# Performance work log

Hardware: AMD Instinct MI355X
Metric: run time of the kernel (lower is better)

## Reference

```python
import jax, jax.numpy as jnp
import numpy as np

N = 8192
F_IN = 256
F_OUT = 128
ALPHA = 0.2  # leaky relu negative slope


def _leaky(x):
    return jnp.where(x >= 0, x, ALPHA * x)


def setup_inputs() -> dict:
    key = jax.random.key(0)
    ks = jax.random.split(key, 12)
    nodes = jax.random.normal(ks[0], (N, F_IN), dtype=jnp.float32)
    adj = (jax.random.uniform(ks[1], (N, N)) < 0.05).astype(jnp.float32)
    adj = jnp.maximum(adj, jnp.eye(N, dtype=jnp.float32))
    s = 0.02
    W1 = jax.random.normal(ks[2], (F_IN, F_OUT), dtype=jnp.float32) * s
    b1 = jnp.zeros((F_OUT,), jnp.float32)
    W2 = jax.random.normal(ks[3], (F_OUT, F_OUT), dtype=jnp.float32) * s
    b2 = jnp.zeros((F_OUT,), jnp.float32)
    W3 = jax.random.normal(ks[4], (F_OUT, F_OUT), dtype=jnp.float32) * s
    b3 = jnp.zeros((F_OUT,), jnp.float32)
    W4 = jax.random.normal(ks[5], (F_OUT, F_OUT), dtype=jnp.float32) * s
    b4 = jnp.zeros((F_OUT,), jnp.float32)
    a_w = jax.random.normal(ks[6], (2 * F_OUT,), dtype=jnp.float32) * s
    a_b = jnp.zeros((), jnp.float32)
    return {"nodes": nodes, "adj": adj, "W1": W1, "b1": b1, "W2": W2, "b2": b2,
            "W3": W3, "b3": b3, "W4": W4, "b4": b4, "a_w": a_w, "a_b": a_b}


def reference(nodes, adj, W1, b1, W2, b2, W3, b3, W4, b4, a_w, a_b):
    # 4-layer linear stack
    h = jax.nn.relu(nodes @ W1 + b1)
    h = jax.nn.relu(h @ W2 + b2)
    h = jax.nn.relu(h @ W3 + b3)
    h = h @ W4 + b4  # (N, F_OUT)
    # a([h_i, h_j]) is linear -> split into src/dst components instead of
    # materializing the (N, N, 2F) repeat+cat tensor; identical math.
    a1, a2 = a_w[:F_OUT], a_w[F_OUT:]
    s_src = h @ a1  # (N,)
    s_dst = h @ a2  # (N,)
    e = _leaky(s_src[:, None] + s_dst[None, :] + a_b)  # (N, N)
    e = jnp.where(adj >= 0.5, e, -jnp.inf)
    attention = jax.nn.softmax(e, axis=1)
    # dropout is identity in eval mode
    return _leaky(attention @ h)  # (N, F_OUT)
```

## Files before the change

### kernel.cpp

```cpp
#include <hip/hip_runtime.h>
#include <hip/hip_bf16.h>

#define N_NODES 8192
#define F_IN    256
#define F_OUT   128
#define CHUNK   512
#define NCH     4
#define CCAP    768

typedef float f4v __attribute__((ext_vector_type(4)));

__device__ __forceinline__ float leaky(float x) { return x >= 0.f ? x : 0.2f * x; }

__global__ __launch_bounds__(256) void mlp_fused(
    const float* __restrict__ nodes,
    const float* __restrict__ W1, const float* __restrict__ b1,
    const float* __restrict__ W2, const float* __restrict__ b2,
    const float* __restrict__ W3, const float* __restrict__ b3,
    const float* __restrict__ W4, const float* __restrict__ b4,
    const float* __restrict__ aw,
    float* __restrict__ h_out, float* __restrict__ ss, float* __restrict__ sd) {
  __shared__ float As[32][36];
  __shared__ float Ws[32][128];
  __shared__ float hTa[128][36];
  __shared__ float hTb[128][36];
  __shared__ float awS[2 * F_OUT];
  __shared__ float sred[2][8][32];

  const int tid = threadIdx.x;
  const int bm0 = blockIdx.x * 32;
  const int mt = tid >> 5;
  const int nt = tid & 31;
  const int ar = tid >> 3;
  const int ac = tid & 7;

  awS[tid] = aw[tid];

  float acc[4][4] = {};

  for (int k0 = 0; k0 < F_IN; k0 += 32) {
    const float4 av = *(const float4*)(nodes + (size_t)(bm0 + ar) * F_IN + k0 + ac * 4);
    float4 wv[4];
#pragma unroll
    for (int i = 0; i < 4; ++i) {
      const int kk = i * 8 + (tid >> 5);
      wv[i] = *(const float4*)(W1 + (size_t)(k0 + kk) * F_OUT + nt * 4);
    }
    __syncthreads();
    As[ac * 4 + 0][ar] = av.x;
    As[ac * 4 + 1][ar] = av.y;
    As[ac * 4 + 2][ar] = av.z;
    As[ac * 4 + 3][ar] = av.w;
#pragma unroll
    for (int i = 0; i < 4; ++i) {
      const int kk = i * 8 + (tid >> 5);
      *(float4*)&Ws[kk][nt * 4] = wv[i];
    }
    __syncthreads();
#pragma unroll
    for (int k = 0; k < 32; ++k) {
      const float4 a = *(const float4*)&As[k][mt * 4];
      const float4 w = *(const float4*)&Ws[k][nt * 4];
      acc[0][0] += a.x * w.x; acc[0][1] += a.x * w.y; acc[0][2] += a.x * w.z; acc[0][3] += a.x * w.w;
      acc[1][0] += a.y * w.x; acc[1][1] += a.y * w.y; acc[1][2] += a.y * w.z; acc[1][3] += a.y * w.w;
      acc[2][0] += a.z * w.x; acc[2][1] += a.z * w.y; acc[2][2] += a.z * w.z; acc[2][3] += a.z * w.w;
      acc[3][0] += a.w * w.x; acc[3][1] += a.w * w.y; acc[3][2] += a.w * w.z; acc[3][3] += a.w * w.w;
    }
  }
  {
    const float4 bv = *(const float4*)(b1 + nt * 4);
#pragma unroll
    for (int i = 0; i < 4; ++i) {
      hTa[nt * 4 + 0][mt * 4 + i] = fmaxf(acc[i][0] + bv.x, 0.f);
      hTa[nt * 4 + 1][mt * 4 + i] = fmaxf(acc[i][1] + bv.y, 0.f);
      hTa[nt * 4 + 2][mt * 4 + i] = fmaxf(acc[i][2] + bv.z, 0.f);
      hTa[nt * 4 + 3][mt * 4 + i] = fmaxf(acc[i][3] + bv.w, 0.f);
    }
  }

  const float* Wl[3] = {W2, W3, W4};
  const float* bl[3] = {b2, b3, b4};
  float* hin = &hTa[0][0];
  float* hout = &hTb[0][0];
  for (int l = 0; l < 3; ++l) {
#pragma unroll
    for (int i = 0; i < 4; ++i)
#pragma unroll
      for (int j = 0; j < 4; ++j) acc[i][j] = 0.f;
    for (int k0 = 0; k0 < F_OUT; k0 += 32) {
      float4 wv[4];
#pragma unroll
      for (int i = 0; i < 4; ++i) {
        const int kk = i * 8 + (tid >> 5);
        wv[i] = *(const float4*)(Wl[l] + (size_t)(k0 + kk) * F_OUT + nt * 4);
      }
      __syncthreads();
#pragma unroll
      for (int i = 0; i < 4; ++i) {
        const int kk = i * 8 + (tid >> 5);
        *(float4*)&Ws[kk][nt * 4] = wv[i];
      }
      __syncthreads();
#pragma unroll
      for (int k = 0; k < 32; ++k) {
        const float4 a = *(const float4*)(hin + (size_t)(k0 + k) * 36 + mt * 4);
        const float4 w = *(const float4*)&Ws[k][nt * 4];
        acc[0][0] += a.x * w.x; acc[0][1] += a.x * w.y; acc[0][2] += a.x * w.z; acc[0][3] += a.x * w.w;
        acc[1][0] += a.y * w.x; acc[1][1] += a.y * w.y; acc[1][2] += a.y * w.z; acc[1][3] += a.y * w.w;
        acc[2][0] += a.z * w.x; acc[2][1] += a.z * w.y; acc[2][2] += a.z * w.z; acc[2][3] += a.z * w.w;
        acc[3][0] += a.w * w.x; acc[3][1] += a.w * w.y; acc[3][2] += a.w * w.z; acc[3][3] += a.w * w.w;
      }
    }
    const float4 bv = *(const float4*)(bl[l] + nt * 4);
    const bool relu = (l < 2);
#pragma unroll
    for (int i = 0; i < 4; ++i) {
      float o0 = acc[i][0] + bv.x, o1 = acc[i][1] + bv.y;
      float o2 = acc[i][2] + bv.z, o3 = acc[i][3] + bv.w;
      if (relu) {
        o0 = fmaxf(o0, 0.f); o1 = fmaxf(o1, 0.f);
        o2 = fmaxf(o2, 0.f); o3 = fmaxf(o3, 0.f);
      }
      hout[(size_t)(nt * 4 + 0) * 36 + mt * 4 + i] = o0;
      hout[(size_t)(nt * 4 + 1) * 36 + mt * 4 + i] = o1;
      hout[(size_t)(nt * 4 + 2) * 36 + mt * 4 + i] = o2;
      hout[(size_t)(nt * 4 + 3) * 36 + mt * 4 + i] = o3;
    }
    float* t = hin; hin = hout; hout = t;
  }
  __syncthreads();

  {
    const int r = tid & 31;
    const int fg = tid >> 5;
    float s1 = 0.f, s2 = 0.f;
#pragma unroll
    for (int i = 0; i < 16; ++i) {
      const int f = fg * 16 + i;
      const float hv = hin[(size_t)f * 36 + r];
      s1 += hv * awS[f];
      s2 += hv * awS[F_OUT + f];
    }
    sred[0][fg][r] = s1;
    sred[1][fg][r] = s2;
  }
  {
    const int r = tid >> 3;
    const int c = tid & 7;
    float4 o[4];
#pragma unroll
    for (int u = 0; u < 4; ++u) {
      o[u].x = hin[(size_t)(c * 16 + u * 4 + 0) * 36 + r];
      o[u].y = hin[(size_t)(c * 16 + u * 4 + 1) * 36 + r];
      o[u].z = hin[(size_t)(c * 16 + u * 4 + 2) * 36 + r];
      o[u].w = hin[(size_t)(c * 16 + u * 4 + 3) * 36 + r];
    }
    float4* dst = (float4*)(h_out + (size_t)(bm0 + r) * F_OUT + c * 16);
#pragma unroll
    for (int u = 0; u < 4; ++u) dst[u] = o[u];
  }
  __syncthreads();
  if (tid < 32) {
    float s1 = 0.f, s2 = 0.f;
#pragma unroll
    for (int g = 0; g < 8; ++g) { s1 += sred[0][g][tid]; s2 += sred[1][g][tid]; }
    ss[bm0 + tid] = s1;
    sd[bm0 + tid] = s2;
  }
}

__global__ __launch_bounds__(512) void attn_kernel(const float* __restrict__ adj,
                                                   const float* __restrict__ h,
                                                   const float* __restrict__ s_src,
                                                   const float* __restrict__ s_dst,
                                                   const float* __restrict__ ab_ptr,
                                                   float* __restrict__ out) {
  __shared__ float2 lst[2][CCAP];
  __shared__ int   cnt[NCH];
  __shared__ float accs[16][32][4];
  __shared__ float red_sum[8];

  const int tid = threadIdx.x;
  const int lane = tid & 63;
  const int wid = tid >> 6;
  const int row = blockIdx.x;
  if (tid < NCH) cnt[tid] = 0;

  const float sbase = s_src[row] + ab_ptr[0];
  const f4v* arow = (const f4v*)(adj + (size_t)row * N_NODES);
  const float4* sd4 = (const float4*)s_dst;
  const float4* h4 = (const float4*)h;
  const unsigned long long lt = (1ull << lane) - 1ull;
  const int g = tid >> 5;
  const int q = tid & 31;

  f4v av = __builtin_nontemporal_load(arow + tid);
  float4 sv = sd4[tid];

  float lsum = 0.f;
  float4 acc = {0.f, 0.f, 0.f, 0.f};
  __syncthreads();

#pragma unroll
  for (int c = 0; c < NCH; ++c) {
    const f4v av_c = av;
    const float4 sv_c = sv;
    if (c + 1 < NCH) {
      av = __builtin_nontemporal_load(arow + (c + 1) * CHUNK + tid);
      sv = sd4[(c + 1) * CHUNK + tid];
    }
    const bool hx = av_c.x >= 0.5f, hy = av_c.y >= 0.5f, hz = av_c.z >= 0.5f, hw = av_c.w >= 0.5f;
    const unsigned long long m0 = __ballot(hx);
    const unsigned long long m1 = __ballot(hy);
    const unsigned long long m2 = __ballot(hz);
    const unsigned long long m3 = __ballot(hw);
    const int t0 = __popcll(m0), t1 = __popcll(m1), t2 = __popcll(m2), t3 = __popcll(m3);
    int wb = 0;
    if (lane == 0) wb = atomicAdd(&cnt[c], t0 + t1 + t2 + t3);
    wb = __shfl(wb, 0, 64);
    const int j0 = (c * CHUNK + tid) * 4;
    float2* lc = lst[c & 1];
    if (hx) {
      const int p = wb + __popcll(m0 & lt);
      if (p < CCAP) { const float w = __expf(leaky(sbase + sv_c.x)); lc[p] = make_float2(w, __int_as_float(j0)); lsum += w; }
    }
    if (hy) {
      const int p = wb + t0 + __popcll(m1 & lt);
      if (p < CCAP) { const float w = __expf(leaky(sbase + sv_c.y)); lc[p] = make_float2(w, __int_as_float(j0 + 1)); lsum += w; }
    }
    if (hz) {
      const int p = wb + t0 + t1 + __popcll(m2 & lt);
      if (p < CCAP) { const float w = __expf(leaky(sbase + sv_c.z)); lc[p] = make_float2(w, __int_as_float(j0 + 2)); lsum += w; }
    }
    if (hw) {
      const int p = wb + t0 + t1 + t2 + __popcll(m3 & lt);
      if (p < CCAP) { const float w = __expf(leaky(sbase + sv_c.w)); lc[p] = make_float2(w, __int_as_float(j0 + 3)); lsum += w; }
    }
    __syncthreads();
    const int n = min(cnt[c], CCAP);
#pragma unroll 2
    for (int p = g; p < n; p += 16) {
      const float2 pr = lc[p];
      const float4 hv = h4[(size_t)__float_as_int(pr.y) * 32 + q];
      acc.x += pr.x * hv.x; acc.y += pr.x * hv.y;
      acc.z += pr.x * hv.z; acc.w += pr.x * hv.w;
    }
  }

#pragma unroll
  for (int o = 1; o < 64; o <<= 1) lsum += __shfl_xor(lsum, o, 64);
  if (lane == 0) red_sum[wid] = lsum;
  *(float4*)&accs[g][q][0] = acc;
  __syncthreads();
  if (tid < 32) {
    float4 t = *(float4*)&accs[0][tid][0];
#pragma unroll
    for (int gg = 1; gg < 16; ++gg) {
      const float4 u = *(float4*)&accs[gg][tid][0];
      t.x += u.x; t.y += u.y; t.z += u.z; t.w += u.w;
    }
    float s = 0.f;
#pragma unroll
    for (int wv = 0; wv < 8; ++wv) s += red_sum[wv];
    const float inv = 1.f / s;
    t.x = leaky(t.x * inv); t.y = leaky(t.y * inv);
    t.z = leaky(t.z * inv); t.w = leaky(t.w * inv);
    ((float4*)out)[(size_t)row * 32 + tid] = t;
  }
}

extern "C" void kernel_launch(void* const* d_in, const int* in_sizes, int n_in,
                              void* d_out, int out_size, void* d_ws, size_t ws_size,
                              hipStream_t stream) {
  const float* nodes = (const float*)d_in[0];
  const float* adj   = (const float*)d_in[1];
  const float* W1    = (const float*)d_in[2];
  const float* b1    = (const float*)d_in[3];
  const float* W2    = (const float*)d_in[4];
  const float* b2    = (const float*)d_in[5];
  const float* W3    = (const float*)d_in[6];
  const float* b3    = (const float*)d_in[7];
  const float* W4    = (const float*)d_in[8];
  const float* b4    = (const float*)d_in[9];
  const float* aw    = (const float*)d_in[10];
  const float* ab    = (const float*)d_in[11];
  float* out = (float*)d_out;

  float* h  = (float*)d_ws;
  float* ss = h + (size_t)N_NODES * F_OUT;
  float* sd = ss + N_NODES;

  mlp_fused<<<N_NODES / 32, 256, 0, stream>>>(nodes, W1, b1, W2, b2, W3, b3,
                                              W4, b4, aw, h, ss, sd);
  attn_kernel<<<N_NODES, 512, 0, stream>>>(adj, h, ss, sd, ab, out);
}
```

Before: 513.1 us.

## Store MLP output in bf16 and gather bf16 rows in attention

The MLP kernel now writes the final hidden features as packed bf16 instead of fp32, and the attention kernel gathers 16-byte bf16 vectors of 8 features each, halving gather bytes per neighbor. The MLP block is reduced to 16 rows per block, doubling the grid size. The attention reduction is reorganized for 32 groups of 16 lanes. This trades precision in h for lower memory traffic in the gather-bound aggregation.

```diff
diff --git a/kernel.cpp b/kernel.cpp
--- a/kernel.cpp
+++ b/kernel.cpp
@@ -4,13 +4,24 @@
 #define N_NODES 8192
 #define F_IN    256
 #define F_OUT   128
+#define BM      16
 #define CHUNK   512
 #define NCH     4
 #define CCAP    768
 
 typedef float f4v __attribute__((ext_vector_type(4)));
+typedef unsigned int u32;
 
 __device__ __forceinline__ float leaky(float x) { return x >= 0.f ? x : 0.2f * x; }
+__device__ __forceinline__ u32 bf16rn(float a) {
+  const u32 u = __float_as_uint(a);
+  return (u + 0x7FFFu + ((u >> 16) & 1u)) >> 16;
+}
+__device__ __forceinline__ u32 packbf(float a, float b) {
+  return bf16rn(a) | (bf16rn(b) << 16);
+}
+__device__ __forceinline__ float bflo(u32 u) { return __uint_as_float(u << 16); }
+__device__ __forceinline__ float bfhi(u32 u) { return __uint_as_float(u & 0xFFFF0000u); }
 
 __global__ __launch_bounds__(256) void mlp_fused(
     const float* __restrict__ nodes,
@@ -19,62 +30,61 @@
     const float* __restrict__ W3, const float* __restrict__ b3,
     const float* __restrict__ W4, const float* __restrict__ b4,
     const float* __restrict__ aw,
-    float* __restrict__ h_out, float* __restrict__ ss, float* __restrict__ sd) {
-  __shared__ float As[32][36];
+    u32* __restrict__ hb_out, float* __restrict__ ss, float* __restrict__ sd) {
+  __shared__ float As[32][18];
   __shared__ float Ws[32][128];
-  __shared__ float hTa[128][36];
-  __shared__ float hTb[128][36];
+  __shared__ float hTa[128][18];
+  __shared__ float hTb[128][18];
   __shared__ float awS[2 * F_OUT];
-  __shared__ float sred[2][8][32];
+  __shared__ float sred[2][16][16];
 
   const int tid = threadIdx.x;
-  const int bm0 = blockIdx.x * 32;
+  const int bm0 = blockIdx.x * BM;
   const int mt = tid >> 5;
   const int nt = tid & 31;
+
+  awS[tid] = aw[tid];
+
+  float acc[2][4] = {};
+
+  const bool al = tid < 128;
   const int ar = tid >> 3;
   const int ac = tid & 7;
-
-  awS[tid] = aw[tid];
-
-  float acc[4][4] = {};
-
   for (int k0 = 0; k0 < F_IN; k0 += 32) {
-    const float4 av = *(const float4*)(nodes + (size_t)(bm0 + ar) * F_IN + k0 + ac * 4);
+    float4 av;
+    if (al) av = *(const float4*)(nodes + (size_t)(bm0 + ar) * F_IN + k0 + ac * 4);
     float4 wv[4];
 #pragma unroll
     for (int i = 0; i < 4; ++i) {
-      const int kk = i * 8 + (tid >> 5);
+      const int kk = i * 8 + mt;
       wv[i] = *(const float4*)(W1 + (size_t)(k0 + kk) * F_OUT + nt * 4);
     }
     __syncthreads();
-    As[ac * 4 + 0][ar] = av.x;
-    As[ac * 4 + 1][ar] = av.y;
-    As[ac * 4 + 2][ar] = av.z;
-    As[ac * 4 + 3][ar] = av.w;
-#pragma unroll
-    for (int i = 0; i < 4; ++i) {
-      const int kk = i * 8 + (tid >> 5);
-      *(float4*)&Ws[kk][nt * 4] = wv[i];
-    }
+    if (al) {
+      As[ac * 4 + 0][ar] = av.x;
+      As[ac * 4 + 1][ar] = av.y;
+      As[ac * 4 + 2][ar] = av.z;
+      As[ac * 4 + 3][ar] = av.w;
+    }
+#pragma unroll
+    for (int i = 0; i < 4; ++i) *(float4*)&Ws[i * 8 + mt][nt * 4] = wv[i];
     __syncthreads();
 #pragma unroll
     for (int k = 0; k < 32; ++k) {
-      const float4 a = *(const float4*)&As[k][mt * 4];
+      const float2 a = *(const float2*)&As[k][mt * 2];
       const float4 w = *(const float4*)&Ws[k][nt * 4];
       acc[0][0] += a.x * w.x; acc[0][1] += a.x * w.y; acc[0][2] += a.x * w.z; acc[0][3] += a.x * w.w;
       acc[1][0] += a.y * w.x; acc[1][1] += a.y * w.y; acc[1][2] += a.y * w.z; acc[1][3] += a.y * w.w;
-      acc[2][0] += a.z * w.x; acc[2][1] += a.z * w.y; acc[2][2] += a.z * w.z; acc[2][3] += a.z * w.w;
-      acc[3][0] += a.w * w.x; acc[3][1] += a.w * w.y; acc[3][2] += a.w * w.z; acc[3][3] += a.w * w.w;
     }
   }
   {
     const float4 bv = *(const float4*)(b1 + nt * 4);
 #pragma unroll
-    for (int i = 0; i < 4; ++i) {
-      hTa[nt * 4 + 0][mt * 4 + i] = fmaxf(acc[i][0] + bv.x, 0.f);
-      hTa[nt * 4 + 1][mt * 4 + i] = fmaxf(acc[i][1] + bv.y, 0.f);
-      hTa[nt * 4 + 2][mt * 4 + i] = fmaxf(acc[i][2] + bv.z, 0.f);
-      hTa[nt * 4 + 3][mt * 4 + i] = fmaxf(acc[i][3] + bv.w, 0.f);
+    for (int i = 0; i < 2; ++i) {
+      hTa[nt * 4 + 0][mt * 2 + i] = fmaxf(acc[i][0] + bv.x, 0.f);
+      hTa[nt * 4 + 1][mt * 2 + i] = fmaxf(acc[i][1] + bv.y, 0.f);
+      hTa[nt * 4 + 2][mt * 2 + i] = fmaxf(acc[i][2] + bv.z, 0.f);
+      hTa[nt * 4 + 3][mt * 2 + i] = fmaxf(acc[i][3] + bv.w, 0.f);
     }
   }
 
@@ -84,60 +94,55 @@
   float* hout = &hTb[0][0];
   for (int l = 0; l < 3; ++l) {
 #pragma unroll
-    for (int i = 0; i < 4; ++i)
+    for (int i = 0; i < 2; ++i)
 #pragma unroll
       for (int j = 0; j < 4; ++j) acc[i][j] = 0.f;
     for (int k0 = 0; k0 < F_OUT; k0 += 32) {
       float4 wv[4];
 #pragma unroll
       for (int i = 0; i < 4; ++i) {
-        const int kk = i * 8 + (tid >> 5);
+        const int kk = i * 8 + mt;
         wv[i] = *(const float4*)(Wl[l] + (size_t)(k0 + kk) * F_OUT + nt * 4);
       }
       __syncthreads();
 #pragma unroll
-      for (int i = 0; i < 4; ++i) {
-        const int kk = i * 8 + (tid >> 5);
-        *(float4*)&Ws[kk][nt * 4] = wv[i];
-      }
+      for (int i = 0; i < 4; ++i) *(float4*)&Ws[i * 8 + mt][nt * 4] = wv[i];
       __syncthreads();
 #pragma unroll
       for (int k = 0; k < 32; ++k) {
-        const float4 a = *(const float4*)(hin + (size_t)(k0 + k) * 36 + mt * 4);
+        const float2 a = *(const float2*)(hin + (size_t)(k0 + k) * 18 + mt * 2);
         const float4 w = *(const float4*)&Ws[k][nt * 4];
         acc[0][0] += a.x * w.x; acc[0][1] += a.x * w.y; acc[0][2] += a.x * w.z; acc[0][3] += a.x * w.w;
         acc[1][0] += a.y * w.x; acc[1][1] += a.y * w.y; acc[1][2] += a.y * w.z; acc[1][3] += a.y * w.w;
-        acc[2][0] += a.z * w.x; acc[2][1] += a.z * w.y; acc[2][2] += a.z * w.z; acc[2][3] += a.z * w.w;
-        acc[3][0] += a.w * w.x; acc[3][1] += a.w * w.y; acc[3][2] += a.w * w.z; acc[3][3] += a.w * w.w;
       }
     }
     const float4 bv = *(const float4*)(bl[l] + nt * 4);
     const bool relu = (l < 2);
 #pragma unroll
-    for (int i = 0; i < 4; ++i) {
+    for (int i = 0; i < 2; ++i) {
       float o0 = acc[i][0] + bv.x, o1 = acc[i][1] + bv.y;
       float o2 = acc[i][2] + bv.z, o3 = acc[i][3] + bv.w;
       if (relu) {
         o0 = fmaxf(o0, 0.f); o1 = fmaxf(o1, 0.f);
         o2 = fmaxf(o2, 0.f); o3 = fmaxf(o3, 0.f);
       }
-      hout[(size_t)(nt * 4 + 0) * 36 + mt * 4 + i] = o0;
-      hout[(size_t)(nt * 4 + 1) * 36 + mt * 4 + i] = o1;
-      hout[(size_t)(nt * 4 + 2) * 36 + mt * 4 + i] = o2;
-      hout[(size_t)(nt * 4 + 3) * 36 + mt * 4 + i] = o3;
+      hout[(size_t)(nt * 4 + 0) * 18 + mt * 2 + i] = o0;
+      hout[(size_t)(nt * 4 + 1) * 18 + mt * 2 + i] = o1;
+      hout[(size_t)(nt * 4 + 2) * 18 + mt * 2 + i] = o2;
+      hout[(size_t)(nt * 4 + 3) * 18 + mt * 2 + i] = o3;
     }
     float* t = hin; hin = hout; hout = t;
   }
   __syncthreads();
 
   {
-    const int r = tid & 31;
-    const int fg = tid >> 5;
+    const int r = tid & 15;
+    const int fg = tid >> 4;
     float s1 = 0.f, s2 = 0.f;
 #pragma unroll
-    for (int i = 0; i < 16; ++i) {
-      const int f = fg * 16 + i;
-      const float hv = hin[(size_t)f * 36 + r];
+    for (int i = 0; i < 8; ++i) {
+      const int f = fg * 8 + i;
+      const float hv = hin[(size_t)f * 18 + r];
       s1 += hv * awS[f];
       s2 += hv * awS[F_OUT + f];
     }
@@ -145,39 +150,35 @@
     sred[1][fg][r] = s2;
   }
   {
-    const int r = tid >> 3;
-    const int c = tid & 7;
-    float4 o[4];
-#pragma unroll
-    for (int u = 0; u < 4; ++u) {
-      o[u].x = hin[(size_t)(c * 16 + u * 4 + 0) * 36 + r];
-      o[u].y = hin[(size_t)(c * 16 + u * 4 + 1) * 36 + r];
-      o[u].z = hin[(size_t)(c * 16 + u * 4 + 2) * 36 + r];
-      o[u].w = hin[(size_t)(c * 16 + u * 4 + 3) * 36 + r];
-    }
-    float4* dst = (float4*)(h_out + (size_t)(bm0 + r) * F_OUT + c * 16);
-#pragma unroll
-    for (int u = 0; u < 4; ++u) dst[u] = o[u];
-  }
-  __syncthreads();
-  if (tid < 32) {
+    const int r = tid >> 4;
+    const int c = tid & 15;
+    const int f0 = c * 8;
+    uint4 o;
+    o.x = packbf(hin[(size_t)(f0 + 0) * 18 + r], hin[(size_t)(f0 + 1) * 18 + r]);
+    o.y = packbf(hin[(size_t)(f0 + 2) * 18 + r], hin[(size_t)(f0 + 3) * 18 + r]);
+    o.z = packbf(hin[(size_t)(f0 + 4) * 18 + r], hin[(size_t)(f0 + 5) * 18 + r]);
+    o.w = packbf(hin[(size_t)(f0 + 6) * 18 + r], hin[(size_t)(f0 + 7) * 18 + r]);
+    ((uint4*)hb_out)[(size_t)(bm0 + r) * 16 + c] = o;
+  }
+  __syncthreads();
+  if (tid < 16) {
     float s1 = 0.f, s2 = 0.f;
 #pragma unroll
-    for (int g = 0; g < 8; ++g) { s1 += sred[0][g][tid]; s2 += sred[1][g][tid]; }
+    for (int g = 0; g < 16; ++g) { s1 += sred[0][g][tid]; s2 += sred[1][g][tid]; }
     ss[bm0 + tid] = s1;
     sd[bm0 + tid] = s2;
   }
 }
 
 __global__ __launch_bounds__(512) void attn_kernel(const float* __restrict__ adj,
-                                                   const float* __restrict__ h,
+                                                   const u32* __restrict__ hb,
                                                    const float* __restrict__ s_src,
                                                    const float* __restrict__ s_dst,
                                                    const float* __restrict__ ab_ptr,
                                                    float* __restrict__ out) {
   __shared__ float2 lst[2][CCAP];
   __shared__ int   cnt[NCH];
-  __shared__ float accs[16][32][4];
+  __shared__ float accs[32][16][8];
   __shared__ float red_sum[8];
 
   const int tid = threadIdx.x;
@@ -189,16 +190,16 @@
   const float sbase = s_src[row] + ab_ptr[0];
   const f4v* arow = (const f4v*)(adj + (size_t)row * N_NODES);
   const float4* sd4 = (const float4*)s_dst;
-  const float4* h4 = (const float4*)h;
+  const uint4* hb4 = (const uint4*)hb;
   const unsigned long long lt = (1ull << lane) - 1ull;
-  const int g = tid >> 5;
-  const int q = tid & 31;
+  const int g = tid >> 4;
+  const int q = tid & 15;
 
   f4v av = __builtin_nontemporal_load(arow + tid);
   float4 sv = sd4[tid];
 
   float lsum = 0.f;
-  float4 acc = {0.f, 0.f, 0.f, 0.f};
+  float accv[8] = {};
   __syncthreads();
 
 #pragma unroll
@@ -239,33 +240,31 @@
     __syncthreads();
     const int n = min(cnt[c], CCAP);
 #pragma unroll 2
-    for (int p = g; p < n; p += 16) {
+    for (int p = g; p < n; p += 32) {
       const float2 pr = lc[p];
-      const float4 hv = h4[(size_t)__float_as_int(pr.y) * 32 + q];
-      acc.x += pr.x * hv.x; acc.y += pr.x * hv.y;
-      acc.z += pr.x * hv.z; acc.w += pr.x * hv.w;
+      const uint4 hv = hb4[(size_t)__float_as_int(pr.y) * 16 + q];
+      accv[0] += pr.x * bflo(hv.x); accv[1] += pr.x * bfhi(hv.x);
+      accv[2] += pr.x * bflo(hv.y); accv[3] += pr.x * bfhi(hv.y);
+      accv[4] += pr.x * bflo(hv.z); accv[5] += pr.x * bfhi(hv.z);
+      accv[6] += pr.x * bflo(hv.w); accv[7] += pr.x * bfhi(hv.w);
     }
   }
 
 #pragma unroll
   for (int o = 1; o < 64; o <<= 1) lsum += __shfl_xor(lsum, o, 64);
   if (lane == 0) red_sum[wid] = lsum;
-  *(float4*)&accs[g][q][0] = acc;
-  __syncthreads();
-  if (tid < 32) {
-    float4 t = *(float4*)&accs[0][tid][0];
-#pragma unroll
-    for (int gg = 1; gg < 16; ++gg) {
-      const float4 u = *(float4*)&accs[gg][tid][0];
-      t.x += u.x; t.y += u.y; t.z += u.z; t.w += u.w;
-    }
+#pragma unroll
+  for (int e = 0; e < 8; ++e) accs[g][q][e] = accv[e];
+  __syncthreads();
+  if (tid < 128) {
+    const int q2 = tid >> 3, e = tid & 7;
     float s = 0.f;
 #pragma unroll
-    for (int wv = 0; wv < 8; ++wv) s += red_sum[wv];
-    const float inv = 1.f / s;
-    t.x = leaky(t.x * inv); t.y = leaky(t.y * inv);
-    t.z = leaky(t.z * inv); t.w = leaky(t.w * inv);
-    ((float4*)out)[(size_t)row * 32 + tid] = t;
+    for (int g2 = 0; g2 < 32; ++g2) s += accs[g2][q2][e];
+    float ws_ = 0.f;
+#pragma unroll
+    for (int wv = 0; wv < 8; ++wv) ws_ += red_sum[wv];
+    out[(size_t)row * F_OUT + tid] = leaky(s / ws_);
   }
 }
 
@@ -286,11 +285,11 @@
   const float* ab    = (const float*)d_in[11];
   float* out = (float*)d_out;
 
-  float* h  = (float*)d_ws;
-  float* ss = h + (size_t)N_NODES * F_OUT;
+  u32*  hb = (u32*)d_ws;
+  float* ss = (float*)((char*)d_ws + (size_t)N_NODES * F_OUT * 2);
   float* sd = ss + N_NODES;
 
-  mlp_fused<<<N_NODES / 32, 256, 0, stream>>>(nodes, W1, b1, W2, b2, W3, b3,
-                                              W4, b4, aw, h, ss, sd);
-  attn_kernel<<<N_NODES, 512, 0, stream>>>(adj, h, ss, sd, ab, out);
-}
+  mlp_fused<<<N_NODES / BM, 256, 0, stream>>>(nodes, W1, b1, W2, b2, W3, b3,
+                                              W4, b4, aw, hb, ss, sd);
+  attn_kernel<<<N_NODES, 512, 0, stream>>>(adj, hb, ss, sd, ab, out);
+}
```

Measured after the change: 465.9 us. 1.1x faster.
